# Kernel tuning notes

Measured on AMD Instinct MI355X. Metric: run time of the kernel, lower is better.

## Reference

```python
import jax, jax.numpy as jnp
import numpy as np

B, L, D, H, K = 32, 2048, 512, 256, 4  # batch, bag_size, input_dim, hidden_dim, n_attentions


def setup_inputs() -> dict:
    key = jax.random.key(0)
    k_x, k1, k1b, k2, k2b, k3, k3b = jax.random.split(key, 7)
    s1 = 1.0 / np.sqrt(D)
    s2 = 1.0 / np.sqrt(H)
    return {
        "x": jax.random.normal(k_x, (B * L, D), dtype=jnp.float32),
        "W1": jax.random.uniform(k1, (D, H), jnp.float32, -s1, s1),
        "b1": jax.random.uniform(k1b, (H,), jnp.float32, -s1, s1),
        "W3": jax.random.uniform(k3, (D, H), jnp.float32, -s1, s1),
        "b3": jax.random.uniform(k3b, (H,), jnp.float32, -s1, s1),
        "W2": jax.random.uniform(k2, (H, K), jnp.float32, -s2, s2),
        "b2": jax.random.uniform(k2b, (K,), jnp.float32, -s2, s2),
        "bag_lengths": jnp.full((B,), L, dtype=jnp.int32),
    }


def reference(x, W1, b1, W3, b3, W2, b2, bag_lengths):
    batch = bag_lengths.shape[0]
    bag = x.shape[0] // batch  # equal-length bags (fast path in original)
    # gated attention MLP, per instance: [N, K]
    A = jnp.tanh(x @ W1 + b1) * jax.nn.sigmoid(x @ W3 + b3)
    A = A @ W2 + b2
    # per-bag softmax over instances, per attention head
    A = A.reshape(batch, bag, K).transpose(0, 2, 1)  # [B, K, L]
    A = jax.nn.softmax(A, axis=2)
    # attention-weighted sum of instances -> [B, K, D] -> [B, K*D]
    out = jnp.einsum('bkl,bld->bkd', A, x.reshape(batch, bag, -1))
    return out.reshape(batch, -1)
```

## Files before the change

kernel.cpp:

```cpp
#include <hip/hip_runtime.h>
#include <hip/hip_bf16.h>


typedef short  bf16x8 __attribute__((ext_vector_type(8)));
typedef float  f32x4  __attribute__((ext_vector_type(4)));

#define D_IN    512
#define H_DIM   256
#define L_BAG   2048

__device__ __forceinline__ short f2bf(float f) {
  union { __hip_bfloat16 h; short s; } u;
  u.h = __float2bfloat16(f);
  return u.s;
}
__device__ __forceinline__ float bf2f(short s) {
  union { float f; unsigned u; } u;
  u.u = ((unsigned)(unsigned short)s) << 16;
  return u.f;
}

__global__ __launch_bounds__(256) void k_prep_w(const float* __restrict__ W1,
                                                const float* __restrict__ W3,
                                                short* __restrict__ wc) {
  int t = blockIdx.x * 256 + threadIdx.x;
  int n_c = t & 511;
  int kc  = t >> 9;
  int kt = kc >> 2, c = kc & 3;
  int g = n_c >> 5, j = n_c & 31;
  const float* src = (j < 16) ? W1 : W3;
  int h = g * 16 + (j & 15);
  bf16x8 v;
  #pragma unroll
  for (int r = 0; r < 8; ++r) v[r] = f2bf(src[(kc * 8 + r) * H_DIM + h]);
  *(bf16x8*)(wc + kt * 16384 + (c * 512 + n_c) * 8) = v;
}

__global__ __launch_bounds__(512, 4) void k_fused(
    const float* __restrict__ x,
    const short* __restrict__ wc,
    const float* __restrict__ b1, const float* __restrict__ b3,
    const float* __restrict__ W2,
    short* __restrict__ part, float* __restrict__ psumP)
{
  __shared__ __align__(16) short xbf[64 * 512];
  __shared__ float lpart[8][64][4];
  __shared__ __align__(16) float wlds[64 * 4];
  __shared__ float psc[4][4];

  const int tid  = threadIdx.x;
  const int lane = tid & 63;
  const int w    = tid >> 6;
  const int l15  = lane & 15;
  const int q    = lane >> 4;
  const int blk  = blockIdx.x;
  const long row0 = (long)blk * 64;

  {
    const int r   = tid & 63;
    const int kc0 = (tid >> 6) * 8;
    const float* xr = x + (row0 + r) * D_IN + kc0 * 8;
    #pragma unroll
    for (int j = 0; j < 8; ++j) {
      float4 f0 = ((const float4*)(xr + j * 8))[0];
      float4 f1 = ((const float4*)(xr + j * 8))[1];
      bf16x8 v;
      v[0] = f2bf(f0.x); v[1] = f2bf(f0.y); v[2] = f2bf(f0.z); v[3] = f2bf(f0.w);
      v[4] = f2bf(f1.x); v[5] = f2bf(f1.y); v[6] = f2bf(f1.z); v[7] = f2bf(f1.w);
      *(bf16x8*)&xbf[((kc0 + j) * 64 + r) * 8] = v;
    }
  }
  __syncthreads();

  f32x4 acc[4][4];
  #pragma unroll
  for (int mf = 0; mf < 4; ++mf)
    #pragma unroll
    for (int nf = 0; nf < 4; ++nf) acc[mf][nf] = (f32x4){0.f, 0.f, 0.f, 0.f};

  const short* bgp = wc + (q * 512 + w * 64 + l15) * 8;

  bf16x8 bp0[2], bp1[2];
#define LDP0(kt) { const short* p_ = bgp + (kt) * 16384; \
    bp0[0] = *(const bf16x8*)(p_);       bp0[1] = *(const bf16x8*)(p_ + 128); }
#define LDP1(kt) { const short* p_ = bgp + (kt) * 16384; \
    bp1[0] = *(const bf16x8*)(p_ + 256); bp1[1] = *(const bf16x8*)(p_ + 384); }

  LDP0(0);
  #pragma unroll
  for (int kt = 0; kt < 16; ++kt) {
    LDP1(kt);
    const int ab = (kt * 4 + q) * 512 + l15 * 8;
    bf16x8 af[4];
    #pragma unroll
    for (int mf = 0; mf < 4; ++mf) af[mf] = *(const bf16x8*)&xbf[ab + mf * 128];
    #pragma unroll
    for (int mf = 0; mf < 4; ++mf) {
      acc[mf][0] = __builtin_amdgcn_mfma_f32_16x16x32_bf16(af[mf], bp0[0], acc[mf][0], 0, 0, 0);
      acc[mf][1] = __builtin_amdgcn_mfma_f32_16x16x32_bf16(af[mf], bp0[1], acc[mf][1], 0, 0, 0);
    }
    if (kt < 15) LDP0(kt + 1);
    #pragma unroll
    for (int mf = 0; mf < 4; ++mf) {
      acc[mf][2] = __builtin_amdgcn_mfma_f32_16x16x32_bf16(af[mf], bp1[0], acc[mf][2], 0, 0, 0);
      acc[mf][3] = __builtin_amdgcn_mfma_f32_16x16x32_bf16(af[mf], bp1[1], acc[mf][3], 0, 0, 0);
    }
  }

  float b1v[2], b3v[2];
  f32x4 wv[2];
  #pragma unroll
  for (int p = 0; p < 2; ++p) {
    int h = w * 32 + p * 16 + l15;
    b1v[p] = b1[h];
    b3v[p] = b3[h];
    wv[p] = *(const f32x4*)&W2[h * 4];
  }
  #pragma unroll
  for (int mf = 0; mf < 4; ++mf) {
    float pl[4][4];
    #pragma unroll
    for (int j = 0; j < 4; ++j)
      #pragma unroll
      for (int kk = 0; kk < 4; ++kk) pl[j][kk] = 0.f;
    #pragma unroll
    for (int p = 0; p < 2; ++p)
      #pragma unroll
      for (int j = 0; j < 4; ++j) {
        float h1 = acc[mf][2 * p][j]     + b1v[p];
        float h3 = acc[mf][2 * p + 1][j] + b3v[p];
        float th = 1.f - __fdividef(2.f, __expf(2.f * h1) + 1.f);
        float sg = __fdividef(1.f, 1.f + __expf(-h3));
        float g = th * sg;
        pl[j][0] += g * wv[p][0];
        pl[j][1] += g * wv[p][1];
        pl[j][2] += g * wv[p][2];
        pl[j][3] += g * wv[p][3];
      }
    #pragma unroll
    for (int off = 1; off < 16; off <<= 1)
      #pragma unroll
      for (int j = 0; j < 4; ++j)
        #pragma unroll
        for (int kk = 0; kk < 4; ++kk)
          pl[j][kk] += __shfl_xor(pl[j][kk], off);
    if (l15 == 0) {
      #pragma unroll
      for (int j = 0; j < 4; ++j)
        #pragma unroll
        for (int kk = 0; kk < 4; ++kk)
          lpart[w][mf * 16 + q * 4 + j][kk] = pl[j][kk];
    }
  }
  __syncthreads();

  if (tid < 256) {
    const int r = tid >> 2, kk = tid & 3;
    float lg = 0.f;
    #pragma unroll
    for (int ww = 0; ww < 8; ++ww) lg += lpart[ww][r][kk];
    float e = __expf(lg);
    wlds[r * 4 + kk] = e;
    float v = e;
    #pragma unroll
    for (int o = 4; o < 64; o <<= 1) v += __shfl_xor(v, o);
    if (lane < 4) psc[tid >> 6][lane] = v;
  }
  __syncthreads();
  if (tid < 4) psumP[blk * 4 + tid] = psc[0][tid] + psc[1][tid] + psc[2][tid] + psc[3][tid];

  {
    const int d  = tid;
    const int kc = d >> 3;
    const int e  = d & 7;
    const short* xcol = &xbf[kc * 512 + e];
    float a0 = 0.f, a1 = 0.f, a2 = 0.f, a3 = 0.f;
    #pragma unroll 8
    for (int i = 0; i < 64; ++i) {
      int l = (i + kc) & 63;
      float xf = bf2f(xcol[l * 8]);
      float4 wv4 = *(const float4*)&wlds[l * 4];
      a0 += wv4.x * xf; a1 += wv4.y * xf; a2 += wv4.z * xf; a3 += wv4.w * xf;
    }
    short* pp = part + (long)blk * 2048 + d;
    pp[0]    = f2bf(a0);
    pp[512]  = f2bf(a1);
    pp[1024] = f2bf(a2);
    pp[1536] = f2bf(a3);
  }
}

__global__ __launch_bounds__(256) void k_finalize(const short* __restrict__ part,
                                                  const float* __restrict__ psumP,
                                                  float* __restrict__ out) {
  int idx = blockIdx.x * 256 + threadIdx.x;
  int b = idx >> 11, k = (idx >> 9) & 3, d = idx & 511;
  const short* pb = part + ((long)b * 32) * 2048 + k * 512 + d;
  float s = 0.f, ps = 0.f;
  #pragma unroll
  for (int c = 0; c < 32; ++c) {
    s  += bf2f(pb[c * 2048]);
    ps += psumP[(b * 32 + c) * 4 + k];
  }
  out[idx] = s / ps;
}

extern "C" void kernel_launch(void* const* d_in, const int* in_sizes, int n_in,
                              void* d_out, int out_size, void* d_ws, size_t ws_size,
                              hipStream_t stream) {
  const float* x  = (const float*)d_in[0];
  const float* W1 = (const float*)d_in[1];
  const float* b1 = (const float*)d_in[2];
  const float* W3 = (const float*)d_in[3];
  const float* b3 = (const float*)d_in[4];
  const float* W2 = (const float*)d_in[5];
  float* out = (float*)d_out;

  char* ws = (char*)d_ws;
  short* wc    = (short*)(ws + 0);
  short* part  = (short*)(ws + 524288);
  float* psumP = (float*)(ws + 524288 + 4194304);

  hipLaunchKernelGGL(k_prep_w,   dim3(128),  dim3(256), 0, stream, W1, W3, wc);
  hipLaunchKernelGGL(k_fused,    dim3(1024), dim3(512), 0, stream, x, wc, b1, b3, W2, part, psumP);
  hipLaunchKernelGGL(k_finalize, dim3(256),  dim3(256), 0, stream, part, psumP, out);
}
```

Measured before the change: 86.57 us.

## Make fused kernel persistent over four row tiles with double-buffered x prefetch

The fused kernel now runs 256 blocks, each handling four consecutive 64-row tiles instead of one. The next tile's x is loaded from global memory into registers while the current tile's MFMA and softmax work runs, then converted and written into a second LDS buffer. This hides global load latency behind compute. In exchange it doubles LDS use, adds 16 float4 registers per thread, lowers the occupancy target to 2, and leaves only 256 blocks to cover the machine's compute units.

After: 196.9 us. 2.27x slower.

```diff
diff --git a/kernel.cpp b/kernel.cpp
--- a/kernel.cpp
+++ b/kernel.cpp
@@ -36,14 +36,14 @@
   *(bf16x8*)(wc + kt * 16384 + (c * 512 + n_c) * 8) = v;
 }
 
-__global__ __launch_bounds__(512, 4) void k_fused(
+__global__ __launch_bounds__(512, 2) void k_fused(
     const float* __restrict__ x,
     const short* __restrict__ wc,
     const float* __restrict__ b1, const float* __restrict__ b3,
     const float* __restrict__ W2,
     short* __restrict__ part, float* __restrict__ psumP)
 {
-  __shared__ __align__(16) short xbf[64 * 512];
+  __shared__ __align__(16) short xbf[2][64 * 512];
   __shared__ float lpart[8][64][4];
   __shared__ __align__(16) float wlds[64 * 4];
   __shared__ float psc[4][4];
@@ -54,29 +54,28 @@
   const int l15  = lane & 15;
   const int q    = lane >> 4;
   const int blk  = blockIdx.x;
-  const long row0 = (long)blk * 64;
-
-  {
-    const int r   = tid & 63;
-    const int kc0 = (tid >> 6) * 8;
-    const float* xr = x + (row0 + r) * D_IN + kc0 * 8;
-    #pragma unroll
-    for (int j = 0; j < 8; ++j) {
-      float4 f0 = ((const float4*)(xr + j * 8))[0];
-      float4 f1 = ((const float4*)(xr + j * 8))[1];
-      bf16x8 v;
-      v[0] = f2bf(f0.x); v[1] = f2bf(f0.y); v[2] = f2bf(f0.z); v[3] = f2bf(f0.w);
-      v[4] = f2bf(f1.x); v[5] = f2bf(f1.y); v[6] = f2bf(f1.z); v[7] = f2bf(f1.w);
-      *(bf16x8*)&xbf[((kc0 + j) * 64 + r) * 8] = v;
-    }
-  }
-  __syncthreads();
-
-  f32x4 acc[4][4];
-  #pragma unroll
-  for (int mf = 0; mf < 4; ++mf)
-    #pragma unroll
-    for (int nf = 0; nf < 4; ++nf) acc[mf][nf] = (f32x4){0.f, 0.f, 0.f, 0.f};
+
+  const int r   = tid & 63;
+  const int kc0 = (tid >> 6) * 8;
+
+  float4 xf[16];
+
+#define XLOAD(tile) { \
+    const float* xr_ = x + ((long)(tile) * 64 + r) * D_IN + kc0 * 8; \
+    _Pragma("unroll") \
+    for (int j_ = 0; j_ < 8; ++j_) { \
+      xf[2 * j_]     = ((const float4*)(xr_ + j_ * 8))[0]; \
+      xf[2 * j_ + 1] = ((const float4*)(xr_ + j_ * 8))[1]; } }
+
+#define XWRITE(buf) { \
+    short* xd_ = (short*)&xbf[buf][0]; \
+    _Pragma("unroll") \
+    for (int j_ = 0; j_ < 8; ++j_) { bf16x8 v_; \
+      v_[0] = f2bf(xf[2*j_].x);   v_[1] = f2bf(xf[2*j_].y); \
+      v_[2] = f2bf(xf[2*j_].z);   v_[3] = f2bf(xf[2*j_].w); \
+      v_[4] = f2bf(xf[2*j_+1].x); v_[5] = f2bf(xf[2*j_+1].y); \
+      v_[6] = f2bf(xf[2*j_+1].z); v_[7] = f2bf(xf[2*j_+1].w); \
+      *(bf16x8*)&xd_[((kc0 + j_) * 64 + r) * 8] = v_; } }
 
   const short* bgp = wc + (q * 512 + w * 64 + l15) * 8;
 
@@ -86,107 +85,134 @@
 #define LDP1(kt) { const short* p_ = bgp + (kt) * 16384; \
     bp1[0] = *(const bf16x8*)(p_ + 256); bp1[1] = *(const bf16x8*)(p_ + 384); }
 
-  LDP0(0);
-  #pragma unroll
-  for (int kt = 0; kt < 16; ++kt) {
-    LDP1(kt);
-    const int ab = (kt * 4 + q) * 512 + l15 * 8;
-    bf16x8 af[4];
+  XLOAD(blk * 4);
+  XWRITE(0);
+  __syncthreads();
+
+  #pragma unroll 1
+  for (int i = 0; i < 4; ++i) {
+    const int cur  = i & 1;
+    const int tile = blk * 4 + i;
+    const short* xc = &xbf[cur][0];
+
+    if (i < 3) {
+      XLOAD(tile + 1);
+      __builtin_amdgcn_sched_barrier(0);
+    }
+
+    f32x4 acc[4][4];
     #pragma unroll
-    for (int mf = 0; mf < 4; ++mf) af[mf] = *(const bf16x8*)&xbf[ab + mf * 128];
+    for (int mf = 0; mf < 4; ++mf)
+      #pragma unroll
+      for (int nf = 0; nf < 4; ++nf) acc[mf][nf] = (f32x4){0.f, 0.f, 0.f, 0.f};
+
+    LDP0(0);
     #pragma unroll
-    for (int mf = 0; mf < 4; ++mf) {
-      acc[mf][0] = __builtin_amdgcn_mfma_f32_16x16x32_bf16(af[mf], bp0[0], acc[mf][0], 0, 0, 0);
-      acc[mf][1] = __builtin_amdgcn_mfma_f32_16x16x32_bf16(af[mf], bp0[1], acc[mf][1], 0, 0, 0);
-    }
-    if (kt < 15) LDP0(kt + 1);
-    #pragma unroll
-    for (int mf = 0; mf < 4; ++mf) {
-      acc[mf][2] = __builtin_amdgcn_mfma_f32_16x16x32_bf16(af[mf], bp1[0], acc[mf][2], 0, 0, 0);
-      acc[mf][3] = __builtin_amdgcn_mfma_f32_16x16x32_bf16(af[mf], bp1[1], acc[mf][3], 0, 0, 0);
-    }
-  }
-
-  float b1v[2], b3v[2];
-  f32x4 wv[2];
-  #pragma unroll
-  for (int p = 0; p < 2; ++p) {
-    int h = w * 32 + p * 16 + l15;
-    b1v[p] = b1[h];
-    b3v[p] = b3[h];
-    wv[p] = *(const f32x4*)&W2[h * 4];
-  }
-  #pragma unroll
-  for (int mf = 0; mf < 4; ++mf) {
-    float pl[4][4];
-    #pragma unroll
-    for (int j = 0; j < 4; ++j)
-      #pragma unroll
-      for (int kk = 0; kk < 4; ++kk) pl[j][kk] = 0.f;
-    #pragma unroll
-    for (int p = 0; p < 2; ++p)
-      #pragma unroll
-      for (int j = 0; j < 4; ++j) {
-        float h1 = acc[mf][2 * p][j]     + b1v[p];
-        float h3 = acc[mf][2 * p + 1][j] + b3v[p];
-        float th = 1.f - __fdividef(2.f, __expf(2.f * h1) + 1.f);
-        float sg = __fdividef(1.f, 1.f + __expf(-h3));
-        float g = th * sg;
-        pl[j][0] += g * wv[p][0];
-        pl[j][1] += g * wv[p][1];
-        pl[j][2] += g * wv[p][2];
-        pl[j][3] += g * wv[p][3];
-      }
-    #pragma unroll
-    for (int off = 1; off < 16; off <<= 1)
-      #pragma unroll
-      for (int j = 0; j < 4; ++j)
+    for (int kt = 0; kt < 16; ++kt) {
+      LDP1(kt);
+      const int ab = (kt * 4 + q) * 512 + l15 * 8;
+      bf16x8 af[4];
+      #pragma unroll
+      for (int mf = 0; mf < 4; ++mf) af[mf] = *(const bf16x8*)&xc[ab + mf * 128];
+      #pragma unroll
+      for (int mf = 0; mf < 4; ++mf) {
+        acc[mf][0] = __builtin_amdgcn_mfma_f32_16x16x32_bf16(af[mf], bp0[0], acc[mf][0], 0, 0, 0);
+        acc[mf][1] = __builtin_amdgcn_mfma_f32_16x16x32_bf16(af[mf], bp0[1], acc[mf][1], 0, 0, 0);
+      }
+      if (kt < 15) LDP0(kt + 1);
+      #pragma unroll
+      for (int mf = 0; mf < 4; ++mf) {
+        acc[mf][2] = __builtin_amdgcn_mfma_f32_16x16x32_bf16(af[mf], bp1[0], acc[mf][2], 0, 0, 0);
+        acc[mf][3] = __builtin_amdgcn_mfma_f32_16x16x32_bf16(af[mf], bp1[1], acc[mf][3], 0, 0, 0);
+      }
+    }
+
+    {
+      float b1v[2], b3v[2];
+      f32x4 wv[2];
+      #pragma unroll
+      for (int p = 0; p < 2; ++p) {
+        int h = w * 32 + p * 16 + l15;
+        b1v[p] = b1[h];
+        b3v[p] = b3[h];
+        wv[p] = *(const f32x4*)&W2[h * 4];
+      }
+      #pragma unroll
+      for (int mf = 0; mf < 4; ++mf) {
+        float pl[4][4];
         #pragma unroll
-        for (int kk = 0; kk < 4; ++kk)
-          pl[j][kk] += __shfl_xor(pl[j][kk], off);
-    if (l15 == 0) {
-      #pragma unroll
-      for (int j = 0; j < 4; ++j)
+        for (int j = 0; j < 4; ++j)
+          #pragma unroll
+          for (int kk = 0; kk < 4; ++kk) pl[j][kk] = 0.f;
         #pragma unroll
-        for (int kk = 0; kk < 4; ++kk)
-          lpart[w][mf * 16 + q * 4 + j][kk] = pl[j][kk];
-    }
-  }
-  __syncthreads();
-
-  if (tid < 256) {
-    const int r = tid >> 2, kk = tid & 3;
-    float lg = 0.f;
-    #pragma unroll
-    for (int ww = 0; ww < 8; ++ww) lg += lpart[ww][r][kk];
-    float e = __expf(lg);
-    wlds[r * 4 + kk] = e;
-    float v = e;
-    #pragma unroll
-    for (int o = 4; o < 64; o <<= 1) v += __shfl_xor(v, o);
-    if (lane < 4) psc[tid >> 6][lane] = v;
-  }
-  __syncthreads();
-  if (tid < 4) psumP[blk * 4 + tid] = psc[0][tid] + psc[1][tid] + psc[2][tid] + psc[3][tid];
-
-  {
-    const int d  = tid;
-    const int kc = d >> 3;
-    const int e  = d & 7;
-    const short* xcol = &xbf[kc * 512 + e];
-    float a0 = 0.f, a1 = 0.f, a2 = 0.f, a3 = 0.f;
-    #pragma unroll 8
-    for (int i = 0; i < 64; ++i) {
-      int l = (i + kc) & 63;
-      float xf = bf2f(xcol[l * 8]);
-      float4 wv4 = *(const float4*)&wlds[l * 4];
-      a0 += wv4.x * xf; a1 += wv4.y * xf; a2 += wv4.z * xf; a3 += wv4.w * xf;
-    }
-    short* pp = part + (long)blk * 2048 + d;
-    pp[0]    = f2bf(a0);
-    pp[512]  = f2bf(a1);
-    pp[1024] = f2bf(a2);
-    pp[1536] = f2bf(a3);
+        for (int p = 0; p < 2; ++p)
+          #pragma unroll
+          for (int j = 0; j < 4; ++j) {
+            float h1 = acc[mf][2 * p][j]     + b1v[p];
+            float h3 = acc[mf][2 * p + 1][j] + b3v[p];
+            float th = 1.f - __fdividef(2.f, __expf(2.f * h1) + 1.f);
+            float sg = __fdividef(1.f, 1.f + __expf(-h3));
+            float g = th * sg;
+            pl[j][0] += g * wv[p][0];
+            pl[j][1] += g * wv[p][1];
+            pl[j][2] += g * wv[p][2];
+            pl[j][3] += g * wv[p][3];
+          }
+        #pragma unroll
+        for (int off = 1; off < 16; off <<= 1)
+          #pragma unroll
+          for (int j = 0; j < 4; ++j)
+            #pragma unroll
+            for (int kk = 0; kk < 4; ++kk)
+              pl[j][kk] += __shfl_xor(pl[j][kk], off);
+        if (l15 == 0) {
+          #pragma unroll
+          for (int j = 0; j < 4; ++j)
+            #pragma unroll
+            for (int kk = 0; kk < 4; ++kk)
+              lpart[w][mf * 16 + q * 4 + j][kk] = pl[j][kk];
+        }
+      }
+    }
+    __syncthreads();
+
+    if (tid < 256) {
+      const int rr = tid >> 2, kk = tid & 3;
+      float lg = 0.f;
+      #pragma unroll
+      for (int ww = 0; ww < 8; ++ww) lg += lpart[ww][rr][kk];
+      float e = __expf(lg);
+      wlds[rr * 4 + kk] = e;
+      float v = e;
+      #pragma unroll
+      for (int o = 4; o < 64; o <<= 1) v += __shfl_xor(v, o);
+      if (lane < 4) psc[tid >> 6][lane] = v;
+    }
+    __syncthreads();
+    if (tid < 4) psumP[tile * 4 + tid] = psc[0][tid] + psc[1][tid] + psc[2][tid] + psc[3][tid];
+
+    {
+      const int d  = tid;
+      const int kc = d >> 3;
+      const int e  = d & 7;
+      const short* xcol = &xc[kc * 512 + e];
+      float a0 = 0.f, a1 = 0.f, a2 = 0.f, a3 = 0.f;
+      #pragma unroll 8
+      for (int ii = 0; ii < 64; ++ii) {
+        int l = (ii + kc) & 63;
+        float xv = bf2f(xcol[l * 8]);
+        float4 wv4 = *(const float4*)&wlds[l * 4];
+        a0 += wv4.x * xv; a1 += wv4.y * xv; a2 += wv4.z * xv; a3 += wv4.w * xv;
+      }
+      short* pp = part + (long)tile * 2048 + d;
+      pp[0]    = f2bf(a0);
+      pp[512]  = f2bf(a1);
+      pp[1024] = f2bf(a2);
+      pp[1536] = f2bf(a3);
+    }
+
+    if (i < 3) XWRITE(cur ^ 1);
+    __syncthreads();
   }
 }
 
@@ -221,7 +247,7 @@
   short* part  = (short*)(ws + 524288);
   float* psumP = (float*)(ws + 524288 + 4194304);
 
-  hipLaunchKernelGGL(k_prep_w,   dim3(128),  dim3(256), 0, stream, W1, W3, wc);
-  hipLaunchKernelGGL(k_fused,    dim3(1024), dim3(512), 0, stream, x, wc, b1, b3, W2, part, psumP);
-  hipLaunchKernelGGL(k_finalize, dim3(256),  dim3(256), 0, stream, part, psumP, out);
-}
+  hipLaunchKernelGGL(k_prep_w,   dim3(128), dim3(256), 0, stream, W1, W3, wc);
+  hipLaunchKernelGGL(k_fused,    dim3(256), dim3(512), 0, stream, x, wc, b1, b3, W2, part, psumP);
+  hipLaunchKernelGGL(k_finalize, dim3(256), dim3(256), 0, stream, part, psumP, out);
+}
```
